# Kernel tuning notes

Measured on AMD Instinct MI355X. Metric: run time of the kernel, lower is better.

## Reference

```python
import jax, jax.numpy as jnp
import numpy as np

NUM_CLASSES = 345
EPS = 1e-12  # torch F.normalize eps


def setup_inputs() -> dict:
    key = jax.random.key(0)
    k1, k2, k3, k4 = jax.random.split(key, 4)
    B, D, N, C = 65536, 512, 34500, NUM_CLASSES
    z = jax.random.normal(k1, (B, D), dtype=jnp.float32)
    supports = jax.random.normal(k2, (N, D), dtype=jnp.float32)
    ent = jax.random.uniform(k3, (N,), dtype=jnp.float32)
    y_hat = jax.random.randint(k4, (N,), 0, C, dtype=jnp.int32)
    return {"z": z, "supports": supports, "ent": ent, "y_hat": y_hat, "filter_K": 100}


def reference(z, supports, ent, y_hat, filter_K):
    # Per-class top-filter_K selection by lowest entropy, expressed as a mask:
    # globally stable-sort by entropy, then per-class running count via one-hot cumsum.
    C = NUM_CLASSES
    order = jnp.argsort(ent)                      # stable sort -> matches per-class torch.sort tie-break
    y_sorted = y_hat[order]                       # [N]
    onehot = jax.nn.one_hot(y_sorted, C, dtype=z.dtype)  # [N, C]
    # rank (1-based, within own class) of each sorted support
    rank = jnp.sum(jnp.cumsum(onehot, axis=0) * onehot, axis=1)  # [N]
    sel = (rank <= filter_K).astype(z.dtype)      # [N] selection mask

    sup = supports[order]                         # [N, D]
    sup = sup / jnp.maximum(jnp.linalg.norm(sup, axis=1, keepdims=True), EPS)  # row-normalize
    # weights = selected_supports^T @ selected_labels (selection folded into mask)
    weights = jnp.einsum('nd,nc->dc', sup, onehot * sel[:, None])  # [D, C]
    weights = weights / jnp.maximum(jnp.linalg.norm(weights, axis=0, keepdims=True), EPS)
    return z @ weights                            # [B, C]
```

## Files before the change

### kernel.cpp

```cpp
#include <hip/hip_runtime.h>
#include <hip/hip_bf16.h>

#define NCLS 345
#define CPAD 384
#define DIM  512
#define BCAP 256

typedef float f32x4 __attribute__((ext_vector_type(4)));
typedef short s16x8 __attribute__((ext_vector_type(8)));
typedef short s16x4 __attribute__((ext_vector_type(4)));
typedef unsigned long long u64;

__device__ __forceinline__ short f2bf(float f) {
  union { float f; unsigned u; } v; v.f = f;
  unsigned r = v.u + 0x7fffu + ((v.u >> 16) & 1u);
  return (short)(r >> 16);
}

__global__ __launch_bounds__(256) void scan_classes(
    const float* __restrict__ ent, const int* __restrict__ y_hat,
    u64* __restrict__ bucket, int* __restrict__ cnt, int N)
{
  int i = blockIdx.x * 256 + threadIdx.x;
  if (i >= N) return;
  int c = y_hat[i];
  unsigned eb = __float_as_uint(ent[i]);
  u64 key = ((u64)eb << 32) | (unsigned)i;
  int p = atomicAdd(&cnt[c], 1);
  if (p < BCAP) bucket[(size_t)c * BCAP + p] = key;
}

__global__ __launch_bounds__(512) void select_accum(
    const float* __restrict__ supports, const u64* __restrict__ bucket,
    const int* __restrict__ cnt, const int* __restrict__ fKp,
    short* __restrict__ Wp)
{
  const int c = blockIdx.x;
  const int tid = threadIdx.x;
  const int lane = tid & 63, w = tid >> 6;
  __shared__ u64   s_key[BCAP];
  __shared__ int   s_selidx[BCAP];
  __shared__ int   s_nsel;
  __shared__ float s_part[8][DIM];
  __shared__ float s_red[8];
  if (tid == 0) s_nsel = 0;
  const int S = (c < NCLS) ? min(cnt[c], BCAP) : 0;
  const int K = fKp[0];
  for (int e = tid; e < S; e += 512) s_key[e] = bucket[(size_t)c * BCAP + e];
  __syncthreads();
  for (int e = tid; e < S; e += 512) {
    u64 ke = s_key[e];
    int r = 0;
    for (int j = 0; j < S; ++j) r += (s_key[j] < ke) ? 1 : 0;
    if (r < K) { int p = atomicAdd(&s_nsel, 1); s_selidx[p] = (int)(unsigned)(ke & 0xffffffffull); }
  }
  __syncthreads();
  const int nsel = s_nsel;
  f32x4 p0 = {0.f,0.f,0.f,0.f}, p1 = {0.f,0.f,0.f,0.f};
  for (int e0 = w; e0 < nsel; e0 += 16) {
    const int e1 = e0 + 8;
    const bool h1 = (e1 < nsel);
    const f32x4* r0 = (const f32x4*)(supports + (size_t)s_selidx[e0] * DIM);
    f32x4 a0 = r0[lane], a1 = r0[lane + 64];
    f32x4 b0 = {0.f,0.f,0.f,0.f}, b1 = {0.f,0.f,0.f,0.f};
    if (h1) {
      const f32x4* r1 = (const f32x4*)(supports + (size_t)s_selidx[e1] * DIM);
      b0 = r1[lane]; b1 = r1[lane + 64];
    }
    float s0 = 0.f, s1 = 0.f;
#pragma unroll
    for (int j = 0; j < 4; ++j) {
      s0 = fmaf(a0[j], a0[j], s0); s0 = fmaf(a1[j], a1[j], s0);
      s1 = fmaf(b0[j], b0[j], s1); s1 = fmaf(b1[j], b1[j], s1);
    }
#pragma unroll
    for (int off = 32; off; off >>= 1) { s0 += __shfl_xor(s0, off); s1 += __shfl_xor(s1, off); }
    float c0 = 1.f / fmaxf(sqrtf(s0), 1e-12f);
    float c1 = 1.f / fmaxf(sqrtf(s1), 1e-12f);
#pragma unroll
    for (int j = 0; j < 4; ++j) { p0[j] = fmaf(a0[j], c0, p0[j]); p1[j] = fmaf(a1[j], c0, p1[j]); }
    if (h1) {
#pragma unroll
      for (int j = 0; j < 4; ++j) { p0[j] = fmaf(b0[j], c1, p0[j]); p1[j] = fmaf(b1[j], c1, p1[j]); }
    }
  }
  *(f32x4*)&s_part[w][lane * 4]       = p0;
  *(f32x4*)&s_part[w][256 + lane * 4] = p1;
  __syncthreads();
  float acc = 0.f;
#pragma unroll
  for (int ww = 0; ww < 8; ++ww) acc += s_part[ww][tid];
  float sq = acc * acc;
#pragma unroll
  for (int off = 32; off; off >>= 1) sq += __shfl_xor(sq, off);
  if (lane == 0) s_red[w] = sq;
  __syncthreads();
  float tot = 0.f;
#pragma unroll
  for (int ww = 0; ww < 8; ++ww) tot += s_red[ww];
  float sc = 1.f / fmaxf(sqrtf(tot), 1e-12f);
  {
    const int k = tid;
    const int kt = k >> 5, fq = (k >> 3) & 3, j = k & 7;
    const int ct = c >> 4, fr = c & 15;
    const size_t pos = (size_t)(kt * 24 + ct) * 512 + fq * 128 + fr * 8 + j;
    Wp[pos] = f2bf(acc * sc);
  }
}

__global__ __launch_bounds__(512, 4) void gemm_zw(
    const float* __restrict__ z, const short* __restrict__ Wp,
    float* __restrict__ out)
{
  __shared__ __align__(16) char lds[65536];
  const int tid  = threadIdx.x;
  const int lane = tid & 63;
  const int w    = tid >> 6;
  const int fr   = lane & 15, fq = lane >> 4;
  const int Mbase = blockIdx.x * 64;

#pragma unroll
  for (int i = 0; i < 8; ++i) {
    const int row = i * 8 + w;
    const char* src = (const char*)(z + (size_t)(Mbase + row) * DIM);
    f32x4 u0 = *(const f32x4*)(src + lane * 32);
    f32x4 u1 = *(const f32x4*)(src + lane * 32 + 16);
    s16x8 b;
#pragma unroll
    for (int j = 0; j < 4; ++j) { b[j] = f2bf(u0[j]); b[4 + j] = f2bf(u1[j]); }
    const int t  = lane >> 2, sfq = lane & 3;
    const int mt = row >> 4,  fr16 = row & 15;
    const unsigned slot = (unsigned)((sfq * 16 + fr16) ^ (t & 15));
    *(s16x8*)(lds + (size_t)(mt * 16 + t) * 1024 + slot * 16) = b;
  }
  __syncthreads();

  const char* pb = (const char*)Wp + (size_t)w * 3 * 1024 + (size_t)lane * 16;

  f32x4 acc[4][3];
#pragma unroll
  for (int mt = 0; mt < 4; ++mt)
#pragma unroll
    for (int nt = 0; nt < 3; ++nt) acc[mt][nt] = f32x4{0.f, 0.f, 0.f, 0.f};

  s16x8 Bbuf[4][3];
#pragma unroll
  for (int s = 0; s < 3; ++s)
#pragma unroll
    for (int nt = 0; nt < 3; ++nt)
      Bbuf[s][nt] = *(const s16x8*)(pb + (size_t)s * 24576 + nt * 1024);

#pragma unroll
  for (int t = 0; t < 16; ++t) {
    if (t + 3 < 16) {
#pragma unroll
      for (int nt = 0; nt < 3; ++nt)
        Bbuf[(t + 3) & 3][nt] = *(const s16x8*)(pb + (size_t)(t + 3) * 24576 + nt * 1024);
    }
    const unsigned rslot = (unsigned)(((fq * 16 + fr) ^ (t & 15)) * 16);
    s16x8 af[4];
#pragma unroll
    for (int mt = 0; mt < 4; ++mt)
      af[mt] = *(const s16x8*)(lds + (size_t)(mt * 16 + t) * 1024 + rslot);
    __builtin_amdgcn_s_setprio(1);
#pragma unroll
    for (int nt = 0; nt < 3; ++nt)
#pragma unroll
      for (int mt = 0; mt < 4; ++mt)
        acc[mt][nt] = __builtin_amdgcn_mfma_f32_16x16x32_bf16(Bbuf[t & 3][nt], af[mt], acc[mt][nt], 0, 0, 0);
    __builtin_amdgcn_s_setprio(0);
  }

#pragma unroll
  for (int h = 0; h < 2; ++h) {
    __syncthreads();
#pragma unroll
    for (int ml = 0; ml < 2; ++ml) {
      const int mt = h * 2 + ml;
      const int rl = ml * 16 + fr;
#pragma unroll
      for (int nt = 0; nt < 3; ++nt) {
        const int colb = w * 48 + nt * 16 + fq * 4;
#pragma unroll
        for (int j = 0; j < 4; ++j) {
          const int col = colb + j;
          if (col < NCLS)
            *(float*)(lds + (((size_t)rl * NCLS + col) << 2)) = acc[mt][nt][j];
        }
      }
    }
    __syncthreads();
    char* dst = (char*)(out + (size_t)(Mbase + h * 32) * NCLS);
    for (int c = tid; c < 2760; c += 512) {
      f32x4 v = *(const f32x4*)(lds + c * 16);
      __builtin_nontemporal_store(v, (f32x4*)(dst + c * 16));
    }
  }
}

extern "C" void kernel_launch(void* const* d_in, const int* in_sizes, int n_in,
                              void* d_out, int out_size, void* d_ws, size_t ws_size,
                              hipStream_t stream) {
  const float* z        = (const float*)d_in[0];
  const float* supports = (const float*)d_in[1];
  const float* ent      = (const float*)d_in[2];
  const int*   y_hat    = (const int*)d_in[3];
  const int*   fK       = (const int*)d_in[4];
  float* out = (float*)d_out;
  short* Wp  = (short*)d_ws;
  const int N = in_sizes[2];
  const int M = in_sizes[0] / DIM;

  const size_t offC = (size_t)CPAD * DIM * 2;
  const size_t offB = offC + 2048;
  int* cnt    = (int*)((char*)d_ws + offC);
  u64* bucket = (u64*)((char*)d_ws + offB);
  hipMemsetAsync(cnt, 0, CPAD * sizeof(int), stream);
  scan_classes<<<dim3((N + 255) / 256), dim3(256), 0, stream>>>(ent, y_hat, bucket, cnt, N);
  select_accum<<<dim3(CPAD), dim3(512), 0, stream>>>(supports, bucket, cnt, fK, Wp);
  gemm_zw<<<dim3(M / 64), dim3(512), 0, stream>>>(z, Wp, out);
}
```

Before: 78.12 us.

## Persistent 4-tile GEMM blocks with double-buffered z staging and direct output stores

The z@W GEMM now has each block process four 64-row tiles. The next tile's z rows are prefetched into registers while MFMAs run on the current tile, then converted and written into a second LDS buffer. Output is stored directly from the accumulators as 16-byte nontemporal writes, with a scalar tail for the last columns, instead of being staged through LDS. This trades occupancy (launch bounds of 1 block per CU, 128 KB of LDS, 256 blocks instead of 1024) and extra register pressure for overlap of global loads with compute and fewer barriers.

New measurement: 168.8 us. 2.16x slower.

```diff
diff --git a/kernel.cpp b/kernel.cpp
--- a/kernel.cpp
+++ b/kernel.cpp
@@ -7,8 +7,8 @@
 #define BCAP 256
 
 typedef float f32x4 __attribute__((ext_vector_type(4)));
+typedef float f32x4u __attribute__((ext_vector_type(4), aligned(4)));
 typedef short s16x8 __attribute__((ext_vector_type(8)));
-typedef short s16x4 __attribute__((ext_vector_type(4)));
 typedef unsigned long long u64;
 
 __device__ __forceinline__ short f2bf(float f) {
@@ -108,94 +108,119 @@
   }
 }
 
-__global__ __launch_bounds__(512, 4) void gemm_zw(
+__global__ __launch_bounds__(512, 1) void gemm_zw(
     const float* __restrict__ z, const short* __restrict__ Wp,
     float* __restrict__ out)
 {
-  __shared__ __align__(16) char lds[65536];
+  __shared__ __align__(16) char lds[131072];
   const int tid  = threadIdx.x;
   const int lane = tid & 63;
   const int w    = tid >> 6;
   const int fr   = lane & 15, fq = lane >> 4;
-  const int Mbase = blockIdx.x * 64;
-
-#pragma unroll
-  for (int i = 0; i < 8; ++i) {
-    const int row = i * 8 + w;
-    const char* src = (const char*)(z + (size_t)(Mbase + row) * DIM);
-    f32x4 u0 = *(const f32x4*)(src + lane * 32);
-    f32x4 u1 = *(const f32x4*)(src + lane * 32 + 16);
-    s16x8 b;
-#pragma unroll
-    for (int j = 0; j < 4; ++j) { b[j] = f2bf(u0[j]); b[4 + j] = f2bf(u1[j]); }
-    const int t  = lane >> 2, sfq = lane & 3;
-    const int mt = row >> 4,  fr16 = row & 15;
-    const unsigned slot = (unsigned)((sfq * 16 + fr16) ^ (t & 15));
-    *(s16x8*)(lds + (size_t)(mt * 16 + t) * 1024 + slot * 16) = b;
-  }
+  const int blk  = blockIdx.x;
+  const int Rbase = blk * 256;
+
+  const int st  = lane >> 2, sfq = lane & 3;
+
+#define STAGE_LOAD(BASE)                                                       \
+  {                                                                            \
+    _Pragma("unroll")                                                          \
+    for (int i = 0; i < 8; ++i) {                                              \
+      const int row = i * 8 + w;                                               \
+      const char* src = (const char*)(z + (size_t)((BASE) + row) * DIM);       \
+      sl0[i] = *(const f32x4*)(src + lane * 32);                               \
+      sl1[i] = *(const f32x4*)(src + lane * 32 + 16);                          \
+    }                                                                          \
+  }
+#define STAGE_WRITE(P)                                                         \
+  {                                                                            \
+    _Pragma("unroll")                                                          \
+    for (int i = 0; i < 8; ++i) {                                              \
+      const int row = i * 8 + w;                                               \
+      s16x8 b;                                                                 \
+      _Pragma("unroll")                                                        \
+      for (int j = 0; j < 4; ++j) { b[j] = f2bf(sl0[i][j]); b[4 + j] = f2bf(sl1[i][j]); } \
+      const int mt = row >> 4, fr16 = row & 15;                                \
+      const unsigned slot = (unsigned)((sfq * 16 + fr16) ^ (st & 15));         \
+      *(s16x8*)(lds + (P) * 65536 + (size_t)(mt * 16 + st) * 1024 + slot * 16) = b; \
+    }                                                                          \
+  }
+
+  f32x4 sl0[8], sl1[8];
+  STAGE_LOAD(Rbase);
+  STAGE_WRITE(0);
   __syncthreads();
 
   const char* pb = (const char*)Wp + (size_t)w * 3 * 1024 + (size_t)lane * 16;
 
-  f32x4 acc[4][3];
-#pragma unroll
-  for (int mt = 0; mt < 4; ++mt)
-#pragma unroll
-    for (int nt = 0; nt < 3; ++nt) acc[mt][nt] = f32x4{0.f, 0.f, 0.f, 0.f};
-
-  s16x8 Bbuf[4][3];
-#pragma unroll
-  for (int s = 0; s < 3; ++s)
-#pragma unroll
-    for (int nt = 0; nt < 3; ++nt)
-      Bbuf[s][nt] = *(const s16x8*)(pb + (size_t)s * 24576 + nt * 1024);
-
-#pragma unroll
-  for (int t = 0; t < 16; ++t) {
-    if (t + 3 < 16) {
+#pragma unroll 1
+  for (int c = 0; c < 4; ++c) {
+    const int p = c & 1;
+    const int Mb = Rbase + c * 64;
+    if (c < 3) STAGE_LOAD(Mb + 64);
+
+    f32x4 acc[4][3];
+#pragma unroll
+    for (int mt = 0; mt < 4; ++mt)
+#pragma unroll
+      for (int nt = 0; nt < 3; ++nt) acc[mt][nt] = f32x4{0.f, 0.f, 0.f, 0.f};
+
+    s16x8 Bbuf[4][3];
+#pragma unroll
+    for (int s = 0; s < 3; ++s)
 #pragma unroll
       for (int nt = 0; nt < 3; ++nt)
-        Bbuf[(t + 3) & 3][nt] = *(const s16x8*)(pb + (size_t)(t + 3) * 24576 + nt * 1024);
-    }
-    const unsigned rslot = (unsigned)(((fq * 16 + fr) ^ (t & 15)) * 16);
-    s16x8 af[4];
-#pragma unroll
-    for (int mt = 0; mt < 4; ++mt)
-      af[mt] = *(const s16x8*)(lds + (size_t)(mt * 16 + t) * 1024 + rslot);
-    __builtin_amdgcn_s_setprio(1);
-#pragma unroll
-    for (int nt = 0; nt < 3; ++nt)
+        Bbuf[s][nt] = *(const s16x8*)(pb + (size_t)s * 24576 + nt * 1024);
+
+    const char* pa = lds + p * 65536;
+#pragma unroll
+    for (int t = 0; t < 16; ++t) {
+      if (t + 3 < 16) {
+#pragma unroll
+        for (int nt = 0; nt < 3; ++nt)
+          Bbuf[(t + 3) & 3][nt] = *(const s16x8*)(pb + (size_t)(t + 3) * 24576 + nt * 1024);
+      }
+      const unsigned rslot = (unsigned)(((fq * 16 + fr) ^ (t & 15)) * 16);
+      s16x8 af[4];
 #pragma unroll
       for (int mt = 0; mt < 4; ++mt)
-        acc[mt][nt] = __builtin_amdgcn_mfma_f32_16x16x32_bf16(Bbuf[t & 3][nt], af[mt], acc[mt][nt], 0, 0, 0);
-    __builtin_amdgcn_s_setprio(0);
-  }
-
-#pragma unroll
-  for (int h = 0; h < 2; ++h) {
-    __syncthreads();
-#pragma unroll
-    for (int ml = 0; ml < 2; ++ml) {
-      const int mt = h * 2 + ml;
-      const int rl = ml * 16 + fr;
+        af[mt] = *(const s16x8*)(pa + (size_t)(mt * 16 + t) * 1024 + rslot);
+      __builtin_amdgcn_s_setprio(1);
+#pragma unroll
+      for (int nt = 0; nt < 3; ++nt)
+#pragma unroll
+        for (int mt = 0; mt < 4; ++mt)
+          acc[mt][nt] = __builtin_amdgcn_mfma_f32_16x16x32_bf16(Bbuf[t & 3][nt], af[mt], acc[mt][nt], 0, 0, 0);
+      __builtin_amdgcn_s_setprio(0);
+    }
+
+    if (c < 3) STAGE_WRITE(p ^ 1);
+
+#pragma unroll
+    for (int mt = 0; mt < 4; ++mt) {
+      const int row = Mb + mt * 16 + fr;
+      float* prow = out + (size_t)row * NCLS;
 #pragma unroll
       for (int nt = 0; nt < 3; ++nt) {
         const int colb = w * 48 + nt * 16 + fq * 4;
-#pragma unroll
-        for (int j = 0; j < 4; ++j) {
-          const int col = colb + j;
-          if (col < NCLS)
-            *(float*)(lds + (((size_t)rl * NCLS + col) << 2)) = acc[mt][nt][j];
+        if (colb + 3 < NCLS) {
+          __builtin_nontemporal_store(acc[mt][nt], (f32x4u*)(prow + colb));
+        } else {
+#pragma unroll
+          for (int j = 0; j < 4; ++j)
+            if (colb + j < NCLS) __builtin_nontemporal_store(acc[mt][nt][j], prow + colb + j);
         }
       }
     }
-    __syncthreads();
-    char* dst = (char*)(out + (size_t)(Mbase + h * 32) * NCLS);
-    for (int c = tid; c < 2760; c += 512) {
-      f32x4 v = *(const f32x4*)(lds + c * 16);
-      __builtin_nontemporal_store(v, (f32x4*)(dst + c * 16));
-    }
-  }
+
+    if (c < 3) {
+      asm volatile("s_waitcnt lgkmcnt(0)" ::: "memory");
+      __builtin_amdgcn_sched_barrier(0);
+      __builtin_amdgcn_s_barrier();
+    }
+  }
+#undef STAGE_LOAD
+#undef STAGE_WRITE
 }
 
 extern "C" void kernel_launch(void* const* d_in, const int* in_sizes, int n_in,
@@ -218,5 +243,5 @@
   hipMemsetAsync(cnt, 0, CPAD * sizeof(int), stream);
   scan_classes<<<dim3((N + 255) / 256), dim3(256), 0, stream>>>(ent, y_hat, bucket, cnt, N);
   select_accum<<<dim3(CPAD), dim3(512), 0, stream>>>(supports, bucket, cnt, fK, Wp);
-  gemm_zw<<<dim3(M / 64), dim3(512), 0, stream>>>(z, Wp, out);
-}
+  gemm_zw<<<dim3(M / 256), dim3(512), 0, stream>>>(z, Wp, out);
+}
```

## Warp-specialize GEMM: producer waves stage z tiles while consumer waves compute

Applied to the files above, without the earlier changes.

The z@W GEMM is split into 4 producer waves and 4 consumer waves. Producers convert fp32 z rows to bf16 into a double-buffered 128KB LDS, and consumers run MFMA on the previous tile, with each consumer now covering 96 columns. Each block processes four 64-row tiles (256 rows) in a software pipeline, and results are written directly from registers with per-element nontemporal stores, dropping the LDS-staged coalesced store. The goal is to overlap z loading and conversion with compute. The costs are lower occupancy (2 blocks per CU), a larger register footprint, and less coalesced output writes.

Result: slower. 185.0 us (+136.9%).

```diff
diff --git a/kernel.cpp b/kernel.cpp
--- a/kernel.cpp
+++ b/kernel.cpp
@@ -8,7 +8,6 @@
 
 typedef float f32x4 __attribute__((ext_vector_type(4)));
 typedef short s16x8 __attribute__((ext_vector_type(8)));
-typedef short s16x4 __attribute__((ext_vector_type(4)));
 typedef unsigned long long u64;
 
 __device__ __forceinline__ short f2bf(float f) {
@@ -108,93 +107,100 @@
   }
 }
 
-__global__ __launch_bounds__(512, 4) void gemm_zw(
+__global__ __launch_bounds__(512, 2) void gemm_zw(
     const float* __restrict__ z, const short* __restrict__ Wp,
     float* __restrict__ out)
 {
-  __shared__ __align__(16) char lds[65536];
+  __shared__ __align__(16) char lds[131072];
   const int tid  = threadIdx.x;
   const int lane = tid & 63;
   const int w    = tid >> 6;
+  const int pw   = w & 3;
   const int fr   = lane & 15, fq = lane >> 4;
-  const int Mbase = blockIdx.x * 64;
-
-#pragma unroll
-  for (int i = 0; i < 8; ++i) {
-    const int row = i * 8 + w;
-    const char* src = (const char*)(z + (size_t)(Mbase + row) * DIM);
-    f32x4 u0 = *(const f32x4*)(src + lane * 32);
-    f32x4 u1 = *(const f32x4*)(src + lane * 32 + 16);
-    s16x8 b;
-#pragma unroll
-    for (int j = 0; j < 4; ++j) { b[j] = f2bf(u0[j]); b[4 + j] = f2bf(u1[j]); }
-    const int t  = lane >> 2, sfq = lane & 3;
-    const int mt = row >> 4,  fr16 = row & 15;
-    const unsigned slot = (unsigned)((sfq * 16 + fr16) ^ (t & 15));
-    *(s16x8*)(lds + (size_t)(mt * 16 + t) * 1024 + slot * 16) = b;
-  }
-  __syncthreads();
-
-  const char* pb = (const char*)Wp + (size_t)w * 3 * 1024 + (size_t)lane * 16;
-
-  f32x4 acc[4][3];
-#pragma unroll
-  for (int mt = 0; mt < 4; ++mt)
-#pragma unroll
-    for (int nt = 0; nt < 3; ++nt) acc[mt][nt] = f32x4{0.f, 0.f, 0.f, 0.f};
-
-  s16x8 Bbuf[4][3];
-#pragma unroll
-  for (int s = 0; s < 3; ++s)
-#pragma unroll
-    for (int nt = 0; nt < 3; ++nt)
-      Bbuf[s][nt] = *(const s16x8*)(pb + (size_t)s * 24576 + nt * 1024);
-
-#pragma unroll
-  for (int t = 0; t < 16; ++t) {
-    if (t + 3 < 16) {
-#pragma unroll
-      for (int nt = 0; nt < 3; ++nt)
-        Bbuf[(t + 3) & 3][nt] = *(const s16x8*)(pb + (size_t)(t + 3) * 24576 + nt * 1024);
-    }
-    const unsigned rslot = (unsigned)(((fq * 16 + fr) ^ (t & 15)) * 16);
-    s16x8 af[4];
-#pragma unroll
-    for (int mt = 0; mt < 4; ++mt)
-      af[mt] = *(const s16x8*)(lds + (size_t)(mt * 16 + t) * 1024 + rslot);
-    __builtin_amdgcn_s_setprio(1);
-#pragma unroll
-    for (int nt = 0; nt < 3; ++nt)
-#pragma unroll
-      for (int mt = 0; mt < 4; ++mt)
-        acc[mt][nt] = __builtin_amdgcn_mfma_f32_16x16x32_bf16(Bbuf[t & 3][nt], af[mt], acc[mt][nt], 0, 0, 0);
-    __builtin_amdgcn_s_setprio(0);
-  }
-
-#pragma unroll
-  for (int h = 0; h < 2; ++h) {
-    __syncthreads();
-#pragma unroll
-    for (int ml = 0; ml < 2; ++ml) {
-      const int mt = h * 2 + ml;
-      const int rl = ml * 16 + fr;
-#pragma unroll
-      for (int nt = 0; nt < 3; ++nt) {
-        const int colb = w * 48 + nt * 16 + fq * 4;
-#pragma unroll
-        for (int j = 0; j < 4; ++j) {
-          const int col = colb + j;
-          if (col < NCLS)
-            *(float*)(lds + (((size_t)rl * NCLS + col) << 2)) = acc[mt][nt][j];
+  const int Rbase = blockIdx.x * 256;
+
+  const char* pb = (const char*)Wp + (size_t)pw * 6 * 1024 + (size_t)lane * 16;
+
+#pragma unroll 1
+  for (int ph = 0; ph < 5; ++ph) {
+    if (w >= 4) {
+      if (ph < 4) {
+        char* buf = lds + (size_t)(ph & 1) * 65536;
+        const int Mb = Rbase + ph * 64;
+#pragma unroll
+        for (int i = 0; i < 16; ++i) {
+          const int row = i * 4 + pw;
+          const char* src = (const char*)(z + (size_t)(Mb + row) * DIM);
+          f32x4 u0 = *(const f32x4*)(src + lane * 32);
+          f32x4 u1 = *(const f32x4*)(src + lane * 32 + 16);
+          s16x8 b;
+#pragma unroll
+          for (int j = 0; j < 4; ++j) { b[j] = f2bf(u0[j]); b[4 + j] = f2bf(u1[j]); }
+          const int t  = lane >> 2, sfq = lane & 3;
+          const int mt = row >> 4,  fr16 = row & 15;
+          const unsigned slot = (unsigned)((sfq * 16 + fr16) ^ (t & 15));
+          *(s16x8*)(buf + (size_t)(mt * 16 + t) * 1024 + slot * 16) = b;
         }
       }
-    }
-    __syncthreads();
-    char* dst = (char*)(out + (size_t)(Mbase + h * 32) * NCLS);
-    for (int c = tid; c < 2760; c += 512) {
-      f32x4 v = *(const f32x4*)(lds + c * 16);
-      __builtin_nontemporal_store(v, (f32x4*)(dst + c * 16));
-    }
+    } else if (ph >= 1) {
+      const int C = ph - 1;
+      const char* pa = lds + (size_t)(C & 1) * 65536;
+      const int Mb = Rbase + C * 64;
+      f32x4 acc[4][6];
+#pragma unroll
+      for (int mt = 0; mt < 4; ++mt)
+#pragma unroll
+        for (int nt = 0; nt < 6; ++nt) acc[mt][nt] = f32x4{0.f, 0.f, 0.f, 0.f};
+      s16x8 Bbuf[3][6];
+#pragma unroll
+      for (int s = 0; s < 2; ++s)
+#pragma unroll
+        for (int nt = 0; nt < 6; ++nt)
+          Bbuf[s][nt] = *(const s16x8*)(pb + (size_t)s * 24576 + nt * 1024);
+#pragma unroll
+      for (int t = 0; t < 16; ++t) {
+        if (t + 2 < 16) {
+#pragma unroll
+          for (int nt = 0; nt < 6; ++nt)
+            Bbuf[(t + 2) % 3][nt] = *(const s16x8*)(pb + (size_t)(t + 2) * 24576 + nt * 1024);
+        }
+        const unsigned rslot = (unsigned)(((fq * 16 + fr) ^ (t & 15)) * 16);
+        s16x8 af[4];
+#pragma unroll
+        for (int mt = 0; mt < 4; ++mt)
+          af[mt] = *(const s16x8*)(pa + (size_t)(mt * 16 + t) * 1024 + rslot);
+        __builtin_amdgcn_s_setprio(1);
+#pragma unroll
+        for (int nt = 0; nt < 6; ++nt)
+#pragma unroll
+          for (int mt = 0; mt < 4; ++mt)
+            acc[mt][nt] = __builtin_amdgcn_mfma_f32_16x16x32_bf16(Bbuf[t % 3][nt], af[mt], acc[mt][nt], 0, 0, 0);
+        __builtin_amdgcn_s_setprio(0);
+      }
+#pragma unroll
+      for (int mt = 0; mt < 4; ++mt) {
+        const int row = Mb + mt * 16 + fr;
+        float* prow = out + (size_t)row * NCLS;
+#pragma unroll
+        for (int nt = 0; nt < 6; ++nt) {
+          const int colb = pw * 96 + nt * 16 + fq * 4;
+          if (colb + 3 < NCLS) {
+            f32x4 v = acc[mt][nt];
+            __builtin_nontemporal_store(v[0], prow + colb);
+            __builtin_nontemporal_store(v[1], prow + colb + 1);
+            __builtin_nontemporal_store(v[2], prow + colb + 2);
+            __builtin_nontemporal_store(v[3], prow + colb + 3);
+          } else {
+#pragma unroll
+            for (int j = 0; j < 4; ++j)
+              if (colb + j < NCLS) __builtin_nontemporal_store(acc[mt][nt][j], prow + colb + j);
+          }
+        }
+      }
+    }
+    asm volatile("s_waitcnt lgkmcnt(0)" ::: "memory");
+    __builtin_amdgcn_sched_barrier(0);
+    __builtin_amdgcn_s_barrier();
   }
 }
 
@@ -218,5 +224,5 @@
   hipMemsetAsync(cnt, 0, CPAD * sizeof(int), stream);
   scan_classes<<<dim3((N + 255) / 256), dim3(256), 0, stream>>>(ent, y_hat, bucket, cnt, N);
   select_accum<<<dim3(CPAD), dim3(512), 0, stream>>>(supports, bucket, cnt, fK, Wp);
-  gemm_zw<<<dim3(M / 64), dim3(512), 0, stream>>>(z, Wp, out);
-}
+  gemm_zw<<<dim3(M / 256), dim3(512), 0, stream>>>(z, Wp, out);
+}
```
